# Performance work log

Hardware: AMD Instinct MI355X
Metric: run time of the kernel (lower is better)

The kernel has to match this reference:

```python
import jax, jax.numpy as jnp
import numpy as np

T, B, L, S = 2048, 64, 32, 256
NEG = -1e30  # effective -inf, safe under logaddexp


def setup_inputs() -> dict:
    key = jax.random.key(0)
    k1, k2, k3 = jax.random.split(key, 3)
    inputs = jax.random.normal(k1, (T, B, L), dtype=jnp.float32)
    targets = jax.random.randint(k2, (B, S), 0, L)
    input_lengths = jnp.full((B,), T, dtype=jnp.int32)
    target_lengths = jnp.full((B,), S, dtype=jnp.int32)
    # learned transition matrix (param of ASGLoss); small random for a non-trivial test
    transition = 0.1 * jax.random.normal(k3, (L, L), dtype=jnp.float32)
    return {"transition": transition, "inputs": inputs, "targets": targets,
            "input_lengths": input_lengths, "target_lengths": target_lengths}


def _fcc_scores(transition, inputs, input_lengths):
    # Fully-connected forward: alpha_t[i] = emit_t[i] + logsumexp_j(alpha_{t-1}[j] + trans[i,j])
    alpha0 = inputs[0]  # [B, L]

    def step(alpha, emit):
        new = emit + jax.nn.logsumexp(alpha[:, None, :] + transition[None, :, :], axis=2)
        return new, new

    _, rest = jax.lax.scan(step, alpha0, inputs[1:])
    alphas = jnp.concatenate([alpha0[None], rest], axis=0)  # [T, B, L]
    b = jnp.arange(inputs.shape[1])
    # causal DP: alpha at t = len-1 is exactly the score for that length
    return jax.nn.logsumexp(alphas[input_lengths - 1, b], axis=-1)  # [B]


def _fac_scores(transition, inputs, targets, input_lengths, target_lengths):
    # Force-aligned forward over target positions s:
    # alpha_t[s] = emit_t[tgt_s] + logaddexp(alpha_{t-1}[s] + trans[tgt_s,tgt_s],
    #                                        alpha_{t-1}[s-1] + trans[tgt_s,tgt_{s-1}])
    Tn, Bn, _ = inputs.shape
    Sn = targets.shape[1]
    # gathered emissions for target labels: [T, B, S]
    emit = jnp.take_along_axis(inputs, jnp.broadcast_to(targets[None], (Tn, Bn, Sn)), axis=2)
    self_tr = transition[targets, targets]                       # [B, S] stay score
    prev = jnp.concatenate([targets[:, :1], targets[:, :-1]], 1)
    move_tr = transition[targets, prev]                          # [B, S] move score (s=0 unused)

    alpha0 = jnp.where((jnp.arange(Sn) == 0)[None, :], emit[0], NEG)  # only s=0 at t=0

    def step(alpha, e):
        stay = alpha + self_tr
        moved = jnp.concatenate(
            [jnp.full_like(alpha[:, :1], NEG), alpha[:, :-1] + move_tr[:, 1:]], axis=1)
        new = e + jnp.logaddexp(stay, moved)
        return new, new

    _, rest = jax.lax.scan(step, alpha0, emit[1:])
    alphas = jnp.concatenate([alpha0[None], rest], axis=0)  # [T, B, S]
    b = jnp.arange(Bn)
    return alphas[input_lengths - 1, b, target_lengths - 1]  # [B]


def reference(transition, inputs, targets, input_lengths, target_lengths):
    # original clamps targets to input length; S <= T here so it's a no-op
    fcc = _fcc_scores(transition, inputs, input_lengths)
    fac = _fac_scores(transition, inputs, targets, input_lengths, target_lengths)
    result = fcc - fac  # [B]
    return result.mean()  # reduction='mean'
```

## Files before the change

kernel.cpp:

```cpp
#include <hip/hip_runtime.h>
#include <math.h>

static constexpr int TB = 64;
static constexpr int LL = 32;
static constexpr int SS = 256;
static constexpr int STRIDE_T = TB * LL;

static constexpr int OF_FWD  = 0;
static constexpr int OF_BWD  = 33;
static constexpr int OF_FACF = 2178;
static constexpr int OF_FACB = 2498;
static constexpr int WSB     = 2818;

#define LN2F 0.69314718055994530942f
#define NEGF (-1e30f)

#define BARX() { asm volatile("s_waitcnt lgkmcnt(0)" ::: "memory"); \
                 __builtin_amdgcn_s_barrier(); \
                 asm volatile("" ::: "memory"); }

template<int CTL>
__device__ __forceinline__ float dpp_f(float x, float oldv) {
  return __int_as_float(__builtin_amdgcn_update_dpp(
      __float_as_int(oldv), __float_as_int(x), CTL, 0xF, 0xF, false));
}
template<int M>
__device__ __forceinline__ int rot_i(int x) {
  return __builtin_amdgcn_update_dpp(0, x, 0x120 + M, 0xF, 0xF, false);
}

typedef unsigned uint2v __attribute__((ext_vector_type(2)));
__device__ __forceinline__ float xsum16(float x) {
  uint2v r = __builtin_amdgcn_permlane16_swap(__float_as_uint(x), __float_as_uint(x), false, false);
  return __uint_as_float(r.x) + __uint_as_float(r.y);
}
__device__ __forceinline__ float xsum32(float x) {
  uint2v r = __builtin_amdgcn_permlane32_swap(__float_as_uint(x), __float_as_uint(x), false, false);
  return __uint_as_float(r.x) + __uint_as_float(r.y);
}
__device__ __forceinline__ float bperm(int addr, float src) {
  return __int_as_float(__builtin_amdgcn_ds_bpermute(addr, __float_as_int(src)));
}

template<int M>
struct Calib {
  __device__ static __forceinline__ void run(const float* trans, int lam, int i, float* Ec) {
    Ec[M] = __expf(trans[i * LL + rot_i<M>(lam)]);
    Calib<M + 1>::run(trans, lam, i, Ec);
  }
};
template<> struct Calib<16> {
  __device__ static __forceinline__ void run(const float*, int, int, float*) {}
};
template<int M>
struct CalibT {
  __device__ static __forceinline__ void run(const float* trans, int lam, int i, float* Ec) {
    Ec[M] = __expf(trans[rot_i<M>(lam) * LL + i]);
    CalibT<M + 1>::run(trans, lam, i, Ec);
  }
};
template<> struct CalibT<16> {
  __device__ static __forceinline__ void run(const float*, int, int, float*) {}
};

#define ROT_MUL(DST, SRC, COEF, ROT) \
  asm("v_mul_f32_dpp %0, %1, %2 row_ror:" #ROT " row_mask:0xf bank_mask:0xf" \
      : "=v"(DST) : "v"(SRC), "v"(COEF))
#define ROT_FMAC(ACC, SRC, COEF, ROT) \
  asm("v_fmac_f32_dpp %0, %1, %2 row_ror:" #ROT " row_mask:0xf bank_mask:0xf" \
      : "+v"(ACC) : "v"(SRC), "v"(COEF))

#define STEP16(EC) { \
  float a0 = EC[0] * A, a1, a2, a3; \
  ROT_MUL(a1, A, EC[1], 1); ROT_MUL(a2, A, EC[2], 2); ROT_MUL(a3, A, EC[3], 3); \
  ROT_FMAC(a0, A, EC[4], 4);  ROT_FMAC(a1, A, EC[5], 5); \
  ROT_FMAC(a2, A, EC[6], 6);  ROT_FMAC(a3, A, EC[7], 7); \
  ROT_FMAC(a0, A, EC[8], 8);  ROT_FMAC(a1, A, EC[9], 9); \
  ROT_FMAC(a2, A, EC[10], 10); ROT_FMAC(a3, A, EC[11], 11); \
  ROT_FMAC(a0, A, EC[12], 12); ROT_FMAC(a1, A, EC[13], 13); \
  ROT_FMAC(a2, A, EC[14], 14); ROT_FMAC(a3, A, EC[15], 15); \
  part = (a0 + a1) + (a2 + a3); }


#define FCC_RENORM() { \
  unsigned uu = (unsigned)__builtin_amdgcn_readfirstlane((int)__float_as_uint(A)); \
  int ex = (int)((uu >> 23) & 255) - 127; \
  A = ldexpf(A, -ex); Kt += ex; }

#define FCC_CONSUME8(PB) { \
  float eb[8]; \
  _Pragma("unroll") for (int q = 0; q < 8; ++q) eb[q] = sE[PB][q][(q & 1) ? lam1 : lam2]; \
  { float part; STEP16(Ec1); A = eb[0] * xsum16(part); } \
  { float part; STEP16(Ec2); A = eb[1] * xsum32(part); } \
  { float part; STEP16(Ec1); A = eb[2] * xsum16(part); } \
  { float part; STEP16(Ec2); A = eb[3] * xsum32(part); } \
  { float part; STEP16(Ec1); A = eb[4] * xsum16(part); } \
  { float part; STEP16(Ec2); A = eb[5] * xsum32(part); } \
  { float part; STEP16(Ec1); A = eb[6] * xsum16(part); } \
  { float part; STEP16(Ec2); A = eb[7] * xsum32(part); } \
  FCC_RENORM(); }

#define FCC_TAIL(PB, CNT) { \
  float eb[8]; \
  _Pragma("unroll") for (int q = 0; q < 8; ++q) eb[q] = sE[PB][q][(q & 1) ? lam1 : lam2]; \
  _Pragma("unroll") for (int q = 0; q < 8; ++q) { \
    if (q >= (CNT)) break; \
    if ((q & 1) == 0) { float part; STEP16(Ec1); A = eb[q] * xsum16(part); } \
    else              { float part; STEP16(Ec2); A = eb[q] * xsum32(part); } } }

#define FCC_BWDCON8(PB) { \
  float eb[8]; \
  _Pragma("unroll") for (int q = 0; q < 8; ++q) eb[q] = sE[PB][q][(q & 1) ? lam1 : lam2]; \
  { A *= eb[7]; float part; STEP16(E1T); A = xsum16(part); } \
  { A *= eb[6]; float part; STEP16(E2T); A = xsum32(part); } \
  { A *= eb[5]; float part; STEP16(E1T); A = xsum16(part); } \
  { A *= eb[4]; float part; STEP16(E2T); A = xsum32(part); } \
  { A *= eb[3]; float part; STEP16(E1T); A = xsum16(part); } \
  { A *= eb[2]; float part; STEP16(E2T); A = xsum32(part); } \
  { A *= eb[1]; float part; STEP16(E1T); A = xsum16(part); } \
  { A *= eb[0]; float part; STEP16(E2T); A = xsum32(part); } \
  FCC_RENORM(); }


#define FAC_STEP(E0, E1, E2, E3) { \
  float ap = dpp_f<0x138>(A3, 0.f);  \
  float n0 = (E0) * fmaf(MV0b,  ap, ST[0] * A0); \
  float n1 = (E1) * fmaf(MVl[1], A0, ST[1] * A1); \
  float n2 = (E2) * fmaf(MVl[2], A1, ST[2] * A2); \
  float n3 = (E3) * fmaf(MVl[3], A2, ST[3] * A3); \
  A0 = n0; A1 = n1; A2 = n2; A3 = n3; }

#define FAC_BOUNDARY() { \
  float maxA = fmaxf(fmaxf(A0, A1), fmaxf(A2, A3)); \
  if (maxA > 0.f) { \
    int ex = (int)((__float_as_uint(maxA) >> 23) & 255) - 127; \
    A0 = ldexpf(A0, -ex); A1 = ldexpf(A1, -ex); \
    A2 = ldexpf(A2, -ex); A3 = ldexpf(A3, -ex); \
    m += (float)ex; \
  } \
  float mp = dpp_f<0x138>(m, NEGF); m = (m == NEGF) ? mp : m; \
  mp = dpp_f<0x138>(m, NEGF);       m = (m == NEGF) ? mp : m; \
  mp = dpp_f<0x138>(m, NEGF); \
  float dlt = fminf(mp - m, 50.0f); \
  float Sin = exp2f(dlt); \
  MV0b = MVl[0] * Sin; }

#define FACF_CON8(PB) { \
  float4 Er[8]; \
  _Pragma("unroll") for (int r = 0; r < 8; ++r) Er[r] = sF[PB][r][l]; \
  _Pragma("unroll") for (int r = 0; r < 8; ++r) \
    FAC_STEP(Er[r].x, Er[r].y, Er[r].z, Er[r].w); \
  FAC_BOUNDARY(); }

#define FACF_TAIL(PB, CNT) { \
  float4 Er[8]; \
  _Pragma("unroll") for (int r = 0; r < 8; ++r) Er[r] = sF[PB][r][l]; \
  _Pragma("unroll") for (int r = 0; r < 8; ++r) { \
    if (r >= (CNT)) break; \
    FAC_STEP(Er[r].x, Er[r].y, Er[r].z, Er[r].w); } }

#define FACB_BOUNDARY() { \
  float maxA = fmaxf(fmaxf(A0, A1), fmaxf(A2, A3)); \
  if (maxA > 0.f) { \
    int ex = (int)((__float_as_uint(maxA) >> 23) & 255) - 127; \
    A0 = ldexpf(A0, -ex); A1 = ldexpf(A1, -ex); \
    A2 = ldexpf(A2, -ex); A3 = ldexpf(A3, -ex); \
    m += (float)ex; \
  } \
  float mp = dpp_f<0x130>(m, NEGF); m = (m == NEGF) ? mp : m; \
  mp = dpp_f<0x130>(m, NEGF);       m = (m == NEGF) ? mp : m; \
  mp = dpp_f<0x130>(m, NEGF); \
  float dlt = fminf(mp - m, 50.0f); \
  MVn3b = MVn[3] * exp2f(dlt); }

#define FACB_CON8(PB) { \
  float4 Er[8]; \
  _Pragma("unroll") for (int r = 0; r < 8; ++r) Er[r] = sF[PB][r][l]; \
  _Pragma("unroll") for (int i = 0; i < 8; ++i) { \
    const int q = 7 - i; \
    float en3 = dpp_f<0x130>(Er[q].x, 0.f);  \
    float an  = dpp_f<0x130>(A0, 0.f); \
    float n0 = fmaf(Er[q].y * MVn[0], A1, Er[q].x * ST[0] * A0); \
    float n1 = fmaf(Er[q].z * MVn[1], A2, Er[q].y * ST[1] * A1); \
    float n2 = fmaf(Er[q].w * MVn[2], A3, Er[q].z * ST[2] * A2); \
    float n3 = fmaf(en3 * MVn3b,      an, Er[q].w * ST[3] * A3); \
    A0 = n0; A1 = n1; A2 = n2; A3 = n3; } \
  FACB_BOUNDARY(); }


#define HLD(Q, K) ({ \
  int tt_ = (isfwd ? (1 + 8 * (Q)) : (lenm1 - 8 * (Q) - 7)) + 2 * (K) + rowoff; \
  tt_ = tt_ < 0 ? 0 : (tt_ > lenm1 ? lenm1 : tt_); \
  gpl[(size_t)tt_ * STRIDE_T]; })

#define PROD_FCC(PB, KK, RV) { sE[PB][2 * (KK) + rowoff][lam1] = __expf(RV); }

#define PROD_FAC(PB, KK, RV) { \
  float e_ = __expf(RV); \
  float4 E0_, E1_; \
  E0_.x = bperm(adA[0], e_); E0_.y = bperm(adA[1], e_); \
  E0_.z = bperm(adA[2], e_); E0_.w = bperm(adA[3], e_); \
  E1_.x = bperm(adB[0], e_); E1_.y = bperm(adB[1], e_); \
  E1_.z = bperm(adB[2], e_); E1_.w = bperm(adB[3], e_); \
  sF[PB][2 * (KK)][l]     = E0_; \
  sF[PB][2 * (KK) + 1][l] = E1_; }


extern "C" __global__ __launch_bounds__(192, 1)
void asg_main(const float* __restrict__ trans, const float* __restrict__ inputs,
              const int* __restrict__ targets, const int* __restrict__ ilen,
              const int* __restrict__ tlen, float* __restrict__ ws) {
  const int tid = (int)threadIdx.x;
  const int w = tid >> 6;
  const int l = tid & 63;
  const int lam1 = l & 31;
  const int lam2 = (l & 15) | ((l >> 5) << 4);
  const int rowoff = l >> 5;

  const int role = (int)blockIdx.x >> 6;
  const int b    = (int)blockIdx.x & 63;

  const int len = ilen[b];
  const int lenm1 = len - 1;
  const int Lsteps = lenm1;
  const int nb = (Lsteps / 2) & ~7;
  const int nf = Lsteps - nb;
  const bool isfwd = (role == 0) || (role == 2);
  const int nsteps = isfwd ? nf : nb;
  const int nph = (nsteps + 7) >> 3;

  const float* gpl = inputs + (size_t)b * LL + lam1;
  float* P = ws + (size_t)b * WSB;

  __shared__ float  sE[2][8][32];
  __shared__ float4 sF[2][8][64];

  if (w == 0) {
    __builtin_amdgcn_s_setprio(1);

    if (role == 0) {
      float Ec1[16], Ec2[16];
      Ec1[0] = __expf(trans[lam2 * LL + lam1]);
      Ec2[0] = __expf(trans[lam1 * LL + lam2]);
      Calib<1>::run(trans, lam1, lam2, Ec1);
      Calib<1>::run(trans, lam2, lam1, Ec2);
      float A = __expf(inputs[(size_t)b * LL + lam1]);
      int Kt = 0;
      for (int p = 0; p < nph; p += 2) {
        BARX();
        { const int rem = nsteps - 8 * p;
          if (rem >= 8) { FCC_CONSUME8(0); } else { FCC_TAIL(0, rem); } }
        BARX();
        if (p + 1 < nph) {
          const int rem = nsteps - 8 * (p + 1);
          if (rem >= 8) { FCC_CONSUME8(1); } else { FCC_TAIL(1, rem); }
        }
      }
      const int par = nsteps & 1;
      const int idx = par ? lam2 : lam1;
      const bool wr = par ? ((l & 16) == 0) : (l < 32);
      if (wr) P[OF_FWD + idx] = A;
      if (l == 0) P[OF_FWD + 32] = (float)Kt;

    } else if (role == 1) {
      float E1T[16], E2T[16];
      E1T[0] = __expf(trans[lam1 * LL + lam2]);
      E2T[0] = __expf(trans[lam2 * LL + lam1]);
      CalibT<1>::run(trans, lam1, lam2, E1T);
      CalibT<1>::run(trans, lam2, lam1, E2T);
      float A = 1.f;
      int Kt = 0;
      for (int p = 0; p < nph; p += 2) {
        BARX();
        FCC_BWDCON8(0);
        BARX();
        if (p + 1 < nph) { FCC_BWDCON8(1); }
      }
      if (l < 32) P[OF_BWD + lam1] = A;
      if (l == 0) P[OF_BWD + 32] = (float)Kt;

    } else if (role == 2) {
      int tg[4];
      #pragma unroll
      for (int q = 0; q < 4; ++q) tg[q] = targets[b * SS + 4 * l + q];
      float ST[4], MVl[4];
      #pragma unroll
      for (int q = 0; q < 4; ++q) ST[q] = __expf(trans[tg[q] * LL + tg[q]]);
      MVl[0] = (l == 0) ? 0.f : __expf(trans[tg[0] * LL + targets[b * SS + 4 * l - 1]]);
      #pragma unroll
      for (int q = 1; q < 4; ++q) MVl[q] = __expf(trans[tg[q] * LL + tg[q - 1]]);

      float A0 = (l == 0) ? __expf(inputs[(size_t)b * LL + tg[0]]) : 0.f;
      float A1 = 0.f, A2 = 0.f, A3 = 0.f;
      float m  = (l == 0) ? 0.f : NEGF;
      float MV0b;
      FAC_BOUNDARY();

      for (int p = 0; p < nph; p += 2) {
        BARX();
        { const int rem = nsteps - 8 * p;
          if (rem >= 8) { FACF_CON8(0); } else { FACF_TAIL(0, rem); } }
        BARX();
        if (p + 1 < nph) {
          const int rem = nsteps - 8 * (p + 1);
          if (rem >= 8) { FACF_CON8(1); } else { FACF_TAIL(1, rem); }
        }
      }
      P[OF_FACF + 4 * l + 0] = A0;
      P[OF_FACF + 4 * l + 1] = A1;
      P[OF_FACF + 4 * l + 2] = A2;
      P[OF_FACF + 4 * l + 3] = A3;
      P[OF_FACF + 256 + l]   = m;

    } else {
      const int tl = tlen[b];
      const int fs = tl - 1;
      int tg[4];
      #pragma unroll
      for (int q = 0; q < 4; ++q) tg[q] = targets[b * SS + 4 * l + q];
      float ST[4], MVn[4];
      #pragma unroll
      for (int q = 0; q < 4; ++q) ST[q] = __expf(trans[tg[q] * LL + tg[q]]);
      MVn[0] = __expf(trans[tg[1] * LL + tg[0]]);
      MVn[1] = __expf(trans[tg[2] * LL + tg[1]]);
      MVn[2] = __expf(trans[tg[3] * LL + tg[2]]);
      int tgn3 = (l < 63) ? targets[b * SS + 4 * l + 4] : 0;
      MVn[3] = (l < 63) ? __expf(trans[tgn3 * LL + tg[3]]) : 0.f;

      float A0 = (4 * l + 0 == fs) ? 1.f : 0.f;
      float A1 = (4 * l + 1 == fs) ? 1.f : 0.f;
      float A2 = (4 * l + 2 == fs) ? 1.f : 0.f;
      float A3 = (4 * l + 3 == fs) ? 1.f : 0.f;
      float m  = (l == (fs >> 2)) ? 0.f : NEGF;
      float MVn3b;
      FACB_BOUNDARY();

      for (int p = 0; p < nph; p += 2) {
        BARX();
        FACB_CON8(0);
        BARX();
        if (p + 1 < nph) { FACB_CON8(1); }
      }
      P[OF_FACB + 4 * l + 0] = A0;
      P[OF_FACB + 4 * l + 1] = A1;
      P[OF_FACB + 4 * l + 2] = A2;
      P[OF_FACB + 4 * l + 3] = A3;
      P[OF_FACB + 256 + l]   = m;
    }

  } else {
    const int kh = 2 * (w - 1);
    const bool fac = (role >= 2);
    int adA[4] = {0, 0, 0, 0}, adB[4] = {0, 0, 0, 0};
    if (fac) {
      #pragma unroll
      for (int j = 0; j < 4; ++j) {
        int tg = targets[b * SS + 4 * l + j];
        adA[j] = tg * 4; adB[j] = adA[j] + 128;
      }
    }
    if (nph > 0) {
      float p0a = HLD(0, kh), p0b = HLD(0, kh + 1);
      float sAa = HLD(1, kh), sAb = HLD(1, kh + 1);
      float sBa = HLD(2, kh), sBb = HLD(2, kh + 1);
      if (fac) { PROD_FAC(0, kh, p0a); PROD_FAC(0, kh + 1, p0b); }
      else     { PROD_FCC(0, kh, p0a); PROD_FCC(0, kh + 1, p0b); }

      for (int p = 0; p < nph; p += 2) {
        BARX();
        if (p + 1 < nph) {
          if (fac) { PROD_FAC(1, kh, sAa); PROD_FAC(1, kh + 1, sAb); }
          else     { PROD_FCC(1, kh, sAa); PROD_FCC(1, kh + 1, sAb); }
          sAa = HLD(p + 3, kh); sAb = HLD(p + 3, kh + 1);
        }
        BARX();
        if (p + 2 < nph) {
          if (fac) { PROD_FAC(0, kh, sBa); PROD_FAC(0, kh + 1, sBb); }
          else     { PROD_FCC(0, kh, sBa); PROD_FCC(0, kh + 1, sBb); }
          sBa = HLD(p + 4, kh); sBb = HLD(p + 4, kh + 1);
        }
      }
    }
  }
}


extern "C" __global__ __launch_bounds__(1024)
void asg_combine(const float* __restrict__ ws, float* __restrict__ out) {
  __shared__ float sd[TB];
  const int tid = (int)threadIdx.x;
  const int w = tid >> 6, l = tid & 63;

  for (int k = 0; k < 4; ++k) {
    const int b = w * 4 + k;
    const float* P = ws + (size_t)b * WSB;

    float al = (l < 32) ? P[OF_FWD + l] : 0.f;
    float vv = (l < 32) ? P[OF_BWD + l] : 0.f;
    float s = al * vv;
    #pragma unroll
    for (int mm = 1; mm < 64; mm <<= 1) s += __shfl_xor(s, mm);
    float fcc = __logf(s) + (P[OF_FWD + 32] + P[OF_BWD + 32]) * LN2F;

    float pa = P[OF_FACF + 4 * l + 0] * P[OF_FACB + 4 * l + 0]
             + P[OF_FACF + 4 * l + 1] * P[OF_FACB + 4 * l + 1]
             + P[OF_FACF + 4 * l + 2] * P[OF_FACB + 4 * l + 2]
             + P[OF_FACF + 4 * l + 3] * P[OF_FACB + 4 * l + 3];
    float sc = P[OF_FACF + 256 + l] + P[OF_FACB + 256 + l];
    float Ms = sc;
    #pragma unroll
    for (int mm = 1; mm < 64; mm <<= 1) Ms = fmaxf(Ms, __shfl_xor(Ms, mm));
    float pp = pa * exp2f(sc - Ms);
    #pragma unroll
    for (int mm = 1; mm < 64; mm <<= 1) pp += __shfl_xor(pp, mm);
    float fac = __logf(pp) + Ms * LN2F;

    if (l == 0) sd[b] = fcc - fac;
  }
  __syncthreads();
  if (tid < TB) {
    float d = sd[tid];
    #pragma unroll
    for (int mm = 1; mm < 64; mm <<= 1) d += __shfl_xor(d, mm);
    if (tid == 0) out[0] = d * (1.0f / TB);
  }
}


extern "C" void kernel_launch(void* const* d_in, const int* in_sizes, int n_in,
                              void* d_out, int out_size, void* d_ws, size_t ws_size,
                              hipStream_t stream) {
  const float* trans   = (const float*)d_in[0];
  const float* inputs  = (const float*)d_in[1];
  const int*   targets = (const int*)d_in[2];
  const int*   ilen    = (const int*)d_in[3];
  const int*   tlen    = (const int*)d_in[4];
  float* out = (float*)d_out;
  float* ws  = (float*)d_ws;

  asg_main<<<dim3(4 * TB), dim3(192), 0, stream>>>(trans, inputs, targets, ilen, tlen, ws);
  asg_combine<<<dim3(1), dim3(1024), 0, stream>>>(ws, out);
}
```

Measured before the change: 82.51 us.

## Double phase depth to 16 timesteps with more producer warps and deeper prefetch

Each barrier phase now covers 16 timesteps instead of 8, so the consumer wave crosses half as many block barriers. Each block grows from 192 to 320 threads, giving four producer waves that fill the larger shared buffers, and the global-load prefetch queue gets one more stage. The FCC matrix-vector step splits its accumulation over eight partial sums instead of four to shorten the dependent FMA chain. Renormalisation still runs every 8 steps. The cost is more registers for the larger emission arrays, more shared memory, and more waves per block.

```diff
diff --git a/kernel.cpp b/kernel.cpp
--- a/kernel.cpp
+++ b/kernel.cpp
@@ -71,15 +71,15 @@
       : "+v"(ACC) : "v"(SRC), "v"(COEF))
 
 #define STEP16(EC) { \
-  float a0 = EC[0] * A, a1, a2, a3; \
+  float a0 = EC[0] * A, a1, a2, a3, a4, a5, a6, a7; \
   ROT_MUL(a1, A, EC[1], 1); ROT_MUL(a2, A, EC[2], 2); ROT_MUL(a3, A, EC[3], 3); \
-  ROT_FMAC(a0, A, EC[4], 4);  ROT_FMAC(a1, A, EC[5], 5); \
-  ROT_FMAC(a2, A, EC[6], 6);  ROT_FMAC(a3, A, EC[7], 7); \
-  ROT_FMAC(a0, A, EC[8], 8);  ROT_FMAC(a1, A, EC[9], 9); \
+  ROT_MUL(a4, A, EC[4], 4); ROT_MUL(a5, A, EC[5], 5); ROT_MUL(a6, A, EC[6], 6); \
+  ROT_MUL(a7, A, EC[7], 7); \
+  ROT_FMAC(a0, A, EC[8], 8);   ROT_FMAC(a1, A, EC[9], 9); \
   ROT_FMAC(a2, A, EC[10], 10); ROT_FMAC(a3, A, EC[11], 11); \
-  ROT_FMAC(a0, A, EC[12], 12); ROT_FMAC(a1, A, EC[13], 13); \
-  ROT_FMAC(a2, A, EC[14], 14); ROT_FMAC(a3, A, EC[15], 15); \
-  part = (a0 + a1) + (a2 + a3); }
+  ROT_FMAC(a4, A, EC[12], 12); ROT_FMAC(a5, A, EC[13], 13); \
+  ROT_FMAC(a6, A, EC[14], 14); ROT_FMAC(a7, A, EC[15], 15); \
+  part = ((a0 + a1) + (a2 + a3)) + ((a4 + a5) + (a6 + a7)); }
 
 
 #define FCC_RENORM() { \
@@ -87,38 +87,39 @@
   int ex = (int)((uu >> 23) & 255) - 127; \
   A = ldexpf(A, -ex); Kt += ex; }
 
-#define FCC_CONSUME8(PB) { \
-  float eb[8]; \
-  _Pragma("unroll") for (int q = 0; q < 8; ++q) eb[q] = sE[PB][q][(q & 1) ? lam1 : lam2]; \
-  { float part; STEP16(Ec1); A = eb[0] * xsum16(part); } \
-  { float part; STEP16(Ec2); A = eb[1] * xsum32(part); } \
-  { float part; STEP16(Ec1); A = eb[2] * xsum16(part); } \
-  { float part; STEP16(Ec2); A = eb[3] * xsum32(part); } \
-  { float part; STEP16(Ec1); A = eb[4] * xsum16(part); } \
-  { float part; STEP16(Ec2); A = eb[5] * xsum32(part); } \
-  { float part; STEP16(Ec1); A = eb[6] * xsum16(part); } \
-  { float part; STEP16(Ec2); A = eb[7] * xsum32(part); } \
+#define FCC_STEP_E(Q) { float part; STEP16(Ec1); A = eb[Q] * xsum16(part); }
+#define FCC_STEP_O(Q) { float part; STEP16(Ec2); A = eb[Q] * xsum32(part); }
+
+#define FCC_CONSUME16(PB) { \
+  float eb[16]; \
+  _Pragma("unroll") for (int q = 0; q < 16; ++q) eb[q] = sE[PB][q][(q & 1) ? lam1 : lam2]; \
+  FCC_STEP_E(0); FCC_STEP_O(1); FCC_STEP_E(2); FCC_STEP_O(3); \
+  FCC_STEP_E(4); FCC_STEP_O(5); FCC_STEP_E(6); FCC_STEP_O(7); \
+  FCC_RENORM(); \
+  FCC_STEP_E(8); FCC_STEP_O(9); FCC_STEP_E(10); FCC_STEP_O(11); \
+  FCC_STEP_E(12); FCC_STEP_O(13); FCC_STEP_E(14); FCC_STEP_O(15); \
   FCC_RENORM(); }
 
-#define FCC_TAIL(PB, CNT) { \
-  float eb[8]; \
-  _Pragma("unroll") for (int q = 0; q < 8; ++q) eb[q] = sE[PB][q][(q & 1) ? lam1 : lam2]; \
-  _Pragma("unroll") for (int q = 0; q < 8; ++q) { \
+#define FCC_TAIL16(PB, CNT) { \
+  float eb[16]; \
+  _Pragma("unroll") for (int q = 0; q < 16; ++q) eb[q] = sE[PB][q][(q & 1) ? lam1 : lam2]; \
+  _Pragma("unroll") for (int q = 0; q < 16; ++q) { \
     if (q >= (CNT)) break; \
     if ((q & 1) == 0) { float part; STEP16(Ec1); A = eb[q] * xsum16(part); } \
-    else              { float part; STEP16(Ec2); A = eb[q] * xsum32(part); } } }
-
-#define FCC_BWDCON8(PB) { \
-  float eb[8]; \
-  _Pragma("unroll") for (int q = 0; q < 8; ++q) eb[q] = sE[PB][q][(q & 1) ? lam1 : lam2]; \
-  { A *= eb[7]; float part; STEP16(E1T); A = xsum16(part); } \
-  { A *= eb[6]; float part; STEP16(E2T); A = xsum32(part); } \
-  { A *= eb[5]; float part; STEP16(E1T); A = xsum16(part); } \
-  { A *= eb[4]; float part; STEP16(E2T); A = xsum32(part); } \
-  { A *= eb[3]; float part; STEP16(E1T); A = xsum16(part); } \
-  { A *= eb[2]; float part; STEP16(E2T); A = xsum32(part); } \
-  { A *= eb[1]; float part; STEP16(E1T); A = xsum16(part); } \
-  { A *= eb[0]; float part; STEP16(E2T); A = xsum32(part); } \
+    else              { float part; STEP16(Ec2); A = eb[q] * xsum32(part); } \
+    if (q == 7) { FCC_RENORM(); } } }
+
+#define FCC_BSTEP_A(Q) { A *= eb[Q]; float part; STEP16(E1T); A = xsum16(part); }
+#define FCC_BSTEP_B(Q) { A *= eb[Q]; float part; STEP16(E2T); A = xsum32(part); }
+
+#define FCC_BWDCON16(PB) { \
+  float eb[16]; \
+  _Pragma("unroll") for (int q = 0; q < 16; ++q) eb[q] = sE[PB][q][(q & 1) ? lam1 : lam2]; \
+  FCC_BSTEP_A(15); FCC_BSTEP_B(14); FCC_BSTEP_A(13); FCC_BSTEP_B(12); \
+  FCC_BSTEP_A(11); FCC_BSTEP_B(10); FCC_BSTEP_A(9);  FCC_BSTEP_B(8); \
+  FCC_RENORM(); \
+  FCC_BSTEP_A(7);  FCC_BSTEP_B(6);  FCC_BSTEP_A(5);  FCC_BSTEP_B(4); \
+  FCC_BSTEP_A(3);  FCC_BSTEP_B(2);  FCC_BSTEP_A(1);  FCC_BSTEP_B(0); \
   FCC_RENORM(); }
 
 
@@ -145,19 +146,23 @@
   float Sin = exp2f(dlt); \
   MV0b = MVl[0] * Sin; }
 
-#define FACF_CON8(PB) { \
-  float4 Er[8]; \
-  _Pragma("unroll") for (int r = 0; r < 8; ++r) Er[r] = sF[PB][r][l]; \
+#define FACF_CON16(PB) { \
+  float4 Er[16]; \
+  _Pragma("unroll") for (int r = 0; r < 16; ++r) Er[r] = sF[PB][r][l]; \
   _Pragma("unroll") for (int r = 0; r < 8; ++r) \
     FAC_STEP(Er[r].x, Er[r].y, Er[r].z, Er[r].w); \
+  FAC_BOUNDARY(); \
+  _Pragma("unroll") for (int r = 8; r < 16; ++r) \
+    FAC_STEP(Er[r].x, Er[r].y, Er[r].z, Er[r].w); \
   FAC_BOUNDARY(); }
 
-#define FACF_TAIL(PB, CNT) { \
-  float4 Er[8]; \
-  _Pragma("unroll") for (int r = 0; r < 8; ++r) Er[r] = sF[PB][r][l]; \
-  _Pragma("unroll") for (int r = 0; r < 8; ++r) { \
+#define FACF_TAIL16(PB, CNT) { \
+  float4 Er[16]; \
+  _Pragma("unroll") for (int r = 0; r < 16; ++r) Er[r] = sF[PB][r][l]; \
+  _Pragma("unroll") for (int r = 0; r < 16; ++r) { \
     if (r >= (CNT)) break; \
-    FAC_STEP(Er[r].x, Er[r].y, Er[r].z, Er[r].w); } }
+    FAC_STEP(Er[r].x, Er[r].y, Er[r].z, Er[r].w); \
+    if (r == 7) { FAC_BOUNDARY(); } } }
 
 #define FACB_BOUNDARY() { \
   float maxA = fmaxf(fmaxf(A0, A1), fmaxf(A2, A3)); \
@@ -173,23 +178,28 @@
   float dlt = fminf(mp - m, 50.0f); \
   MVn3b = MVn[3] * exp2f(dlt); }
 
-#define FACB_CON8(PB) { \
-  float4 Er[8]; \
-  _Pragma("unroll") for (int r = 0; r < 8; ++r) Er[r] = sF[PB][r][l]; \
-  _Pragma("unroll") for (int i = 0; i < 8; ++i) { \
-    const int q = 7 - i; \
-    float en3 = dpp_f<0x130>(Er[q].x, 0.f);  \
+#define FACB_STEP(Q) { \
+    float en3 = dpp_f<0x130>(Er[Q].x, 0.f);  \
     float an  = dpp_f<0x130>(A0, 0.f); \
-    float n0 = fmaf(Er[q].y * MVn[0], A1, Er[q].x * ST[0] * A0); \
-    float n1 = fmaf(Er[q].z * MVn[1], A2, Er[q].y * ST[1] * A1); \
-    float n2 = fmaf(Er[q].w * MVn[2], A3, Er[q].z * ST[2] * A2); \
-    float n3 = fmaf(en3 * MVn3b,      an, Er[q].w * ST[3] * A3); \
-    A0 = n0; A1 = n1; A2 = n2; A3 = n3; } \
+    float n0 = fmaf(Er[Q].y * MVn[0], A1, Er[Q].x * ST[0] * A0); \
+    float n1 = fmaf(Er[Q].z * MVn[1], A2, Er[Q].y * ST[1] * A1); \
+    float n2 = fmaf(Er[Q].w * MVn[2], A3, Er[Q].z * ST[2] * A2); \
+    float n3 = fmaf(en3 * MVn3b,      an, Er[Q].w * ST[3] * A3); \
+    A0 = n0; A1 = n1; A2 = n2; A3 = n3; }
+
+#define FACB_CON16(PB) { \
+  float4 Er[16]; \
+  _Pragma("unroll") for (int r = 0; r < 16; ++r) Er[r] = sF[PB][r][l]; \
+  FACB_STEP(15); FACB_STEP(14); FACB_STEP(13); FACB_STEP(12); \
+  FACB_STEP(11); FACB_STEP(10); FACB_STEP(9);  FACB_STEP(8); \
+  FACB_BOUNDARY(); \
+  FACB_STEP(7);  FACB_STEP(6);  FACB_STEP(5);  FACB_STEP(4); \
+  FACB_STEP(3);  FACB_STEP(2);  FACB_STEP(1);  FACB_STEP(0); \
   FACB_BOUNDARY(); }
 
 
 #define HLD(Q, K) ({ \
-  int tt_ = (isfwd ? (1 + 8 * (Q)) : (lenm1 - 8 * (Q) - 7)) + 2 * (K) + rowoff; \
+  int tt_ = (isfwd ? (1 + 16 * (Q)) : (lenm1 - 16 * (Q) - 15)) + 2 * (K) + rowoff; \
   tt_ = tt_ < 0 ? 0 : (tt_ > lenm1 ? lenm1 : tt_); \
   gpl[(size_t)tt_ * STRIDE_T]; })
 
@@ -205,8 +215,12 @@
   sF[PB][2 * (KK)][l]     = E0_; \
   sF[PB][2 * (KK) + 1][l] = E1_; }
 
-
-extern "C" __global__ __launch_bounds__(192, 1)
+#define PRODUCE(PB, VA, VB) { \
+  if (fac) { PROD_FAC(PB, kh, VA); PROD_FAC(PB, kh + 1, VB); } \
+  else     { PROD_FCC(PB, kh, VA); PROD_FCC(PB, kh + 1, VB); } }
+
+
+extern "C" __global__ __launch_bounds__(320, 1)
 void asg_main(const float* __restrict__ trans, const float* __restrict__ inputs,
               const int* __restrict__ targets, const int* __restrict__ ilen,
               const int* __restrict__ tlen, float* __restrict__ ws) {
@@ -223,17 +237,17 @@
   const int len = ilen[b];
   const int lenm1 = len - 1;
   const int Lsteps = lenm1;
-  const int nb = (Lsteps / 2) & ~7;
+  const int nb = (Lsteps / 2) & ~15;
   const int nf = Lsteps - nb;
   const bool isfwd = (role == 0) || (role == 2);
   const int nsteps = isfwd ? nf : nb;
-  const int nph = (nsteps + 7) >> 3;
+  const int nph = (nsteps + 15) >> 4;
 
   const float* gpl = inputs + (size_t)b * LL + lam1;
   float* P = ws + (size_t)b * WSB;
 
-  __shared__ float  sE[2][8][32];
-  __shared__ float4 sF[2][8][64];
+  __shared__ float  sE[2][16][32];
+  __shared__ float4 sF[2][16][64];
 
   if (w == 0) {
     __builtin_amdgcn_s_setprio(1);
@@ -248,12 +262,12 @@
       int Kt = 0;
       for (int p = 0; p < nph; p += 2) {
         BARX();
-        { const int rem = nsteps - 8 * p;
-          if (rem >= 8) { FCC_CONSUME8(0); } else { FCC_TAIL(0, rem); } }
+        { const int rem = nsteps - 16 * p;
+          if (rem >= 16) { FCC_CONSUME16(0); } else { FCC_TAIL16(0, rem); } }
         BARX();
         if (p + 1 < nph) {
-          const int rem = nsteps - 8 * (p + 1);
-          if (rem >= 8) { FCC_CONSUME8(1); } else { FCC_TAIL(1, rem); }
+          const int rem = nsteps - 16 * (p + 1);
+          if (rem >= 16) { FCC_CONSUME16(1); } else { FCC_TAIL16(1, rem); }
         }
       }
       const int par = nsteps & 1;
@@ -272,9 +286,9 @@
       int Kt = 0;
       for (int p = 0; p < nph; p += 2) {
         BARX();
-        FCC_BWDCON8(0);
-        BARX();
-        if (p + 1 < nph) { FCC_BWDCON8(1); }
+        FCC_BWDCON16(0);
+        BARX();
+        if (p + 1 < nph) { FCC_BWDCON16(1); }
       }
       if (l < 32) P[OF_BWD + lam1] = A;
       if (l == 0) P[OF_BWD + 32] = (float)Kt;
@@ -298,12 +312,12 @@
 
       for (int p = 0; p < nph; p += 2) {
         BARX();
-        { const int rem = nsteps - 8 * p;
-          if (rem >= 8) { FACF_CON8(0); } else { FACF_TAIL(0, rem); } }
+        { const int rem = nsteps - 16 * p;
+          if (rem >= 16) { FACF_CON16(0); } else { FACF_TAIL16(0, rem); } }
         BARX();
         if (p + 1 < nph) {
-          const int rem = nsteps - 8 * (p + 1);
-          if (rem >= 8) { FACF_CON8(1); } else { FACF_TAIL(1, rem); }
+          const int rem = nsteps - 16 * (p + 1);
+          if (rem >= 16) { FACF_CON16(1); } else { FACF_TAIL16(1, rem); }
         }
       }
       P[OF_FACF + 4 * l + 0] = A0;
@@ -337,9 +351,9 @@
 
       for (int p = 0; p < nph; p += 2) {
         BARX();
-        FACB_CON8(0);
-        BARX();
-        if (p + 1 < nph) { FACB_CON8(1); }
+        FACB_CON16(0);
+        BARX();
+        if (p + 1 < nph) { FACB_CON16(1); }
       }
       P[OF_FACB + 4 * l + 0] = A0;
       P[OF_FACB + 4 * l + 1] = A1;
@@ -359,26 +373,25 @@
         adA[j] = tg * 4; adB[j] = adA[j] + 128;
       }
     }
-    if (nph > 0) {
-      float p0a = HLD(0, kh), p0b = HLD(0, kh + 1);
-      float sAa = HLD(1, kh), sAb = HLD(1, kh + 1);
-      float sBa = HLD(2, kh), sBb = HLD(2, kh + 1);
-      if (fac) { PROD_FAC(0, kh, p0a); PROD_FAC(0, kh + 1, p0b); }
-      else     { PROD_FCC(0, kh, p0a); PROD_FCC(0, kh + 1, p0b); }
-
-      for (int p = 0; p < nph; p += 2) {
-        BARX();
-        if (p + 1 < nph) {
-          if (fac) { PROD_FAC(1, kh, sAa); PROD_FAC(1, kh + 1, sAb); }
-          else     { PROD_FCC(1, kh, sAa); PROD_FCC(1, kh + 1, sAb); }
-          sAa = HLD(p + 3, kh); sAb = HLD(p + 3, kh + 1);
-        }
-        BARX();
-        if (p + 2 < nph) {
-          if (fac) { PROD_FAC(0, kh, sBa); PROD_FAC(0, kh + 1, sBb); }
-          else     { PROD_FCC(0, kh, sBa); PROD_FCC(0, kh + 1, sBb); }
-          sBa = HLD(p + 4, kh); sBb = HLD(p + 4, kh + 1);
-        }
+    float R1a = HLD(0, kh), R1b = HLD(0, kh + 1);
+    float R2a = HLD(1, kh), R2b = HLD(1, kh + 1);
+    float R3a = HLD(2, kh), R3b = HLD(2, kh + 1);
+    PRODUCE(0, R1a, R1b);
+    R1a = R2a; R1b = R2b; R2a = R3a; R2b = R3b;
+    R3a = HLD(3, kh); R3b = HLD(3, kh + 1);
+
+    for (int p = 0; p < nph; p += 2) {
+      BARX();
+      if (p + 1 < nph) {
+        float Na = HLD(p + 4, kh), Nb = HLD(p + 4, kh + 1);
+        PRODUCE(1, R1a, R1b);
+        R1a = R2a; R1b = R2b; R2a = R3a; R2b = R3b; R3a = Na; R3b = Nb;
+      }
+      BARX();
+      if (p + 2 < nph) {
+        float Na = HLD(p + 5, kh), Nb = HLD(p + 5, kh + 1);
+        PRODUCE(0, R1a, R1b);
+        R1a = R2a; R1b = R2b; R2a = R3a; R2b = R3b; R3a = Na; R3b = Nb;
       }
     }
   }
@@ -438,6 +451,6 @@
   float* out = (float*)d_out;
   float* ws  = (float*)d_ws;
 
-  asg_main<<<dim3(4 * TB), dim3(192), 0, stream>>>(trans, inputs, targets, ilen, tlen, ws);
+  asg_main<<<dim3(4 * TB), dim3(320), 0, stream>>>(trans, inputs, targets, ilen, tlen, ws);
   asg_combine<<<dim3(1), dim3(1024), 0, stream>>>(ws, out);
 }
```

After: 81.91 us. No clear change (-0.7%).
